# Optimization experiments

Measured on AMD Instinct MI355X. Metric: run time of the kernel, lower is better.

The kernel has to match this reference:

```python
import jax, jax.numpy as jnp
import numpy as np

B, S, H = 64, 2048, 1024

def setup_inputs() -> dict:
    key = jax.random.key(0)
    k1, k2, k3, k4, k5 = jax.random.split(key, 5)
    scale = 1.0 / np.sqrt(H)
    return {
        "dec_hidden": jax.random.normal(k1, (B, 1, H), dtype=jnp.float32),
        "enc_outputs": jax.random.normal(k2, (B, S, H), dtype=jnp.float32),
        "W_h": jax.random.normal(k3, (H, H), dtype=jnp.float32) * scale,
        "W_s": jax.random.normal(k4, (H, H), dtype=jnp.float32) * scale,
        "v": jax.random.normal(k5, (H,), dtype=jnp.float32) * scale,
    }

def reference(dec_hidden, enc_outputs, W_h, W_s, v):
    # energy = tanh(enc @ W_h^T + dec @ W_s^T)  -> [B, S, H]
    enc_proj = jnp.einsum('bsh,oh->bso', enc_outputs, W_h)
    dec_proj = jnp.einsum('bqh,oh->bqo', dec_hidden, W_s)  # [B,1,H]
    energy = jnp.tanh(enc_proj + dec_proj)
    # score = energy @ v -> [B, S]
    score = jnp.einsum('bsh,h->bs', energy, v)
    weights = jax.nn.softmax(score, axis=-1)
    # context = weights[:, None, :] @ enc_outputs -> [B, 1, H]
    context = jnp.einsum('bs,bsh->bh', weights, enc_outputs)[:, None, :]
    return (context, weights)
```

## Files before the change

kernel.cpp:

```cpp
#include <hip/hip_runtime.h>
#include <hip/hip_bf16.h>


#define B_ 64
#define S_ 2048
#define H_ 1024
#define NT_ 16

typedef __attribute__((ext_vector_type(8))) short short8;
typedef __attribute__((ext_vector_type(4))) float floatx4;

__device__ __forceinline__ short f2bf(float f) {
    unsigned u = __float_as_uint(f);
    return (short)((u + 0x7FFFu + ((u >> 16) & 1u)) >> 16);
}
__device__ __forceinline__ unsigned pk2bf(float a, float b) {
    unsigned ua = __float_as_uint(a), ub = __float_as_uint(b);
    ua = (ua + 0x7FFFu + ((ua >> 16) & 1u)) >> 16;
    ub = (ub + 0x7FFFu + ((ub >> 16) & 1u)) & 0xFFFF0000u;
    return ua | ub;
}
__device__ __forceinline__ void gload_lds16(const void* g, void* l) {
    __builtin_amdgcn_global_load_lds(
        (const __attribute__((address_space(1))) unsigned*)g,
        (__attribute__((address_space(3))) unsigned*)l, 16, 0, 0);
}

__global__ __launch_bounds__(256) void zero_score_kernel(float* __restrict__ sc) {
    ((float4*)sc)[blockIdx.x * 256 + threadIdx.x] = make_float4(0.f, 0.f, 0.f, 0.f);
}

__global__ __launch_bounds__(256) void dec_proj_kernel(
        const float* __restrict__ dec, const float* __restrict__ Ws,
        float* __restrict__ dp) {
    __shared__ float sdec[H_];
    const int b = blockIdx.y;
    const int o = blockIdx.x * 256 + threadIdx.x;
    ((float4*)sdec)[threadIdx.x] = ((const float4*)(dec + b * H_))[threadIdx.x];
    __syncthreads();
    const float4* wr = (const float4*)(Ws + (size_t)o * H_);
    float acc = 0.f;
#pragma unroll 4
    for (int i = 0; i < H_ / 4; ++i) {
        float4 wv = wr[i];
        acc += sdec[4*i+0]*wv.x + sdec[4*i+1]*wv.y + sdec[4*i+2]*wv.z + sdec[4*i+3]*wv.w;
    }
    dp[b * H_ + o] = acc;
}

__global__ __launch_bounds__(256) void cvt_wh_kernel(
        const float* __restrict__ Wh, short* __restrict__ Wbf) {
    const int i = blockIdx.x * 256 + threadIdx.x;
    float4 f = ((const float4*)Wh)[i];
    *(short4*)&Wbf[i * 4] = make_short4(f2bf(f.x), f2bf(f.y), f2bf(f.z), f2bf(f.w));
}

__global__ __launch_bounds__(256) void cvt_enc_kernel(
        const float* __restrict__ enc, short* __restrict__ out) {
    const size_t total = (size_t)B_ * S_ * H_ / 8;
    for (size_t c = (size_t)blockIdx.x * 256 + threadIdx.x; c < total;
         c += (size_t)gridDim.x * 256) {
        const float4* p = (const float4*)enc + c * 2;
        float4 f0 = p[0], f1 = p[1];
        union { short8 s; unsigned u[4]; } cv;
        cv.u[0] = pk2bf(f0.x, f0.y);
        cv.u[1] = pk2bf(f0.z, f0.w);
        cv.u[2] = pk2bf(f1.x, f1.y);
        cv.u[3] = pk2bf(f1.z, f1.w);
        ((short8*)out)[c] = cv.s;
    }
}

#define STAGEA(bufp, half, ktile) do {                                          \
    gload_lds16(gA + (size_t)(half) * (128 * H_) + (ktile) * 64,                \
                &As[(bufp)][(half)][wave * 512]);                               \
    gload_lds16(gA + (size_t)(half) * (128 * H_) + (ktile) * 64 + 64 * H_,      \
                &As[(bufp)][(half)][4096 + wave * 512]);                        \
} while (0)
#define STAGEB(bufp, half, ktile) do {                                          \
    gload_lds16(gB + (size_t)(half) * (128 * H_) + (ktile) * 64,                \
                &Bs[(bufp)][(half)][wave * 512]);                               \
    gload_lds16(gB + (size_t)(half) * (128 * H_) + (ktile) * 64 + 64 * H_,      \
                &Bs[(bufp)][(half)][4096 + wave * 512]);                        \
} while (0)

#define MFMA16(I0) do {                                                         \
    _Pragma("unroll")                                                           \
    for (int kt = 0; kt < 2; ++kt) {                                            \
        _Pragma("unroll")                                                       \
        for (int j = 0; j < 4; ++j) {                                           \
            acc[I0][j]     = __builtin_amdgcn_mfma_f32_16x16x32_bf16(           \
                                 af[0][kt], bfr[kt][j], acc[I0][j], 0, 0, 0);   \
            acc[(I0)+1][j] = __builtin_amdgcn_mfma_f32_16x16x32_bf16(           \
                                 af[1][kt], bfr[kt][j], acc[(I0)+1][j], 0, 0, 0); \
        }                                                                       \
    }                                                                           \
} while (0)

#define PHASE(I0, STG, TAILWAIT) do {                                           \
    _Pragma("unroll")                                                           \
    for (int ii = 0; ii < 2; ++ii)                                              \
        _Pragma("unroll")                                                       \
        for (int kt = 0; kt < 2; ++kt)                                          \
            af[ii][kt] = *(const short8*)(aBase + ((I0) + ii) * 1024 +          \
                                          (((kt * 4 + quad) ^ swz) * 8));       \
    STG;                                                                        \
    __builtin_amdgcn_s_barrier();                                               \
    asm volatile("s_waitcnt lgkmcnt(0)" ::: "memory");                          \
    __builtin_amdgcn_s_setprio(1);                                              \
    MFMA16(I0);                                                                 \
    __builtin_amdgcn_s_setprio(0);                                              \
    TAILWAIT;                                                                   \
    __builtin_amdgcn_s_barrier();                                               \
} while (0)

__global__ __launch_bounds__(512, 2) void score256_kernel(
        const short* __restrict__ encbf, const short* __restrict__ Wbf,
        const float* __restrict__ dp, const float* __restrict__ v,
        float* __restrict__ score) {
    __shared__ short As[2][2][128 * 64];
    __shared__ short Bs[2][2][128 * 64];

    const int tid  = threadIdx.x;
    const int wave = tid >> 6;
    const int lane = tid & 63;
    const int l15  = lane & 15;
    const int quad = lane >> 4;
    const int wy   = wave & 1;
    const int wx   = wave >> 1;

    const int mtile = blockIdx.x >> 2;
    const int nb    = blockIdx.x & 3;
    const int m0    = mtile * 256;
    const int n0    = nb * 256;
    const int b     = m0 >> 11;
    const int swz   = l15 & 7;

    const int rr0 = tid >> 3;
    const int g8  = (tid & 7) ^ (rr0 & 7);
    const short* gA = encbf + (size_t)(m0 + rr0) * H_ + g8 * 8;
    const short* gB = Wbf   + (size_t)(n0 + rr0) * H_ + g8 * 8;

    floatx4 acc[8][4];
#pragma unroll
    for (int i = 0; i < 8; ++i)
#pragma unroll
        for (int j = 0; j < 4; ++j) acc[i][j] = (floatx4){0.f, 0.f, 0.f, 0.f};

    short8 af[2][2];
    short8 bfr[2][4];

    STAGEA(0, 0, 0); STAGEA(0, 1, 0);
    STAGEB(0, 0, 0); STAGEB(0, 1, 0);
    STAGEB(1, 0, 1); STAGEB(1, 1, 1);
    asm volatile("s_waitcnt vmcnt(4)" ::: "memory");
    __builtin_amdgcn_s_barrier();

#pragma unroll 1
    for (int t = 0; t < NT_; ++t) {
        const int buf = t & 1;
        const short* aBase = &As[buf][wy][0] + l15 * 64;
        const short* bBase = &Bs[buf][wx >> 1][0] + ((wx & 1) * 64 + l15) * 64;

#pragma unroll
        for (int kt = 0; kt < 2; ++kt)
#pragma unroll
            for (int j = 0; j < 4; ++j)
                bfr[kt][j] = *(const short8*)(bBase + j * 1024 +
                                              (((kt * 4 + quad) ^ swz) * 8));

        PHASE(0, { if (t + 1 < NT_) STAGEA(buf ^ 1, 0, t + 1); }, (void)0);
        PHASE(2, { if (t + 1 < NT_) STAGEA(buf ^ 1, 1, t + 1); }, (void)0);
        PHASE(4, { if (t + 2 < NT_) STAGEB(buf, 0, t + 2); }, (void)0);
        PHASE(6, { if (t + 2 < NT_) STAGEB(buf, 1, t + 2); },
              { if (t < NT_ - 2) { asm volatile("s_waitcnt vmcnt(4)" ::: "memory"); }
                else             { asm volatile("s_waitcnt vmcnt(0)" ::: "memory"); } });
    }

    float part[8][4];
#pragma unroll
    for (int i = 0; i < 8; ++i)
#pragma unroll
        for (int r = 0; r < 4; ++r) part[i][r] = 0.f;

#pragma unroll
    for (int j = 0; j < 4; ++j) {
        const int o = n0 + wx * 64 + j * 16 + l15;
        const float dpv = dp[b * H_ + o];
        const float vv  = v[o];
#pragma unroll
        for (int i = 0; i < 8; ++i)
#pragma unroll
            for (int r = 0; r < 4; ++r) {
                float x = acc[i][j][r] + dpv;
                x = fminf(10.f, fmaxf(-10.f, x));
                float e = __expf(x + x);
                float t = 1.f - 2.f * __builtin_amdgcn_rcpf(e + 1.f);
                part[i][r] += t * vv;
            }
    }
#pragma unroll
    for (int i = 0; i < 8; ++i)
#pragma unroll
        for (int r = 0; r < 4; ++r) {
            float s = part[i][r];
            s += __shfl_xor(s, 1, 64);
            s += __shfl_xor(s, 2, 64);
            s += __shfl_xor(s, 4, 64);
            s += __shfl_xor(s, 8, 64);
            if (l15 == 0)
                atomicAdd(&score[m0 + wy * 128 + i * 16 + quad * 4 + r], s);
        }
}

__global__ __launch_bounds__(256, 3) void score_kernel_fb(
        const float* __restrict__ enc, const short* __restrict__ Wbf,
        const float* __restrict__ dp, const float* __restrict__ v,
        float* __restrict__ score) {
    __shared__ short As[128 * 64];
    __shared__ short Bs[128 * 64];

    const int tid  = threadIdx.x;
    const int wave = tid >> 6;
    const int lane = tid & 63;
    const int l15  = lane & 15;
    const int quad = lane >> 4;
    const int wy   = wave & 1;
    const int wx   = wave >> 1;

    const int mtile = blockIdx.x >> 3;
    const int nb    = blockIdx.x & 7;
    const int m0    = mtile * 128;
    const int n0    = nb * 128;
    const int b     = m0 >> 11;

    floatx4 acc[4][4];
#pragma unroll
    for (int i = 0; i < 4; ++i)
#pragma unroll
        for (int j = 0; j < 4; ++j) acc[i][j] = (floatx4){0.f, 0.f, 0.f, 0.f};

    const short* aLds = As + (wy * 64 + l15) * 64;
    const short* bLds = Bs + (wx * 64 + l15) * 64;
    const int swz = l15 & 7;
    const int srow = tid >> 3;
    const int bc   = tid & 7;

    for (int k0 = 0; k0 < H_; k0 += 64) {
#pragma unroll
        for (int r = 0; r < 4; ++r) {
            const int n = r * 32 + srow;
            const int g = bc ^ (n & 7);
            const short* gp = Wbf + (size_t)(n0 + n) * H_ + k0 + g * 8;
            gload_lds16(gp, (void*)(Bs + (r * 256 + wave * 64) * 8));
        }
#pragma unroll
        for (int i = 0; i < 4; ++i) {
            const int La = i * 256 + tid;
            const int m  = La >> 3;
            const int c8 = La & 7;
            const float4* gp = (const float4*)(enc + (size_t)(m0 + m) * H_ + k0 + c8 * 8);
            float4 f0 = gp[0], f1 = gp[1];
            union { short8 s; unsigned u[4]; } cv;
            cv.u[0] = pk2bf(f0.x, f0.y);
            cv.u[1] = pk2bf(f0.z, f0.w);
            cv.u[2] = pk2bf(f1.x, f1.y);
            cv.u[3] = pk2bf(f1.z, f1.w);
            *(short8*)&As[m * 64 + (c8 ^ (m & 7)) * 8] = cv.s;
        }
        __syncthreads();
#pragma unroll
        for (int kt = 0; kt < 2; ++kt) {
            short8 a2[4], b2[4];
#pragma unroll
            for (int i = 0; i < 4; ++i)
                a2[i] = *(const short8*)(aLds + i * 16 * 64 + (((kt * 4 + quad) ^ swz) * 8));
#pragma unroll
            for (int j = 0; j < 4; ++j)
                b2[j] = *(const short8*)(bLds + j * 16 * 64 + (((kt * 4 + quad) ^ swz) * 8));
#pragma unroll
            for (int i = 0; i < 4; ++i)
#pragma unroll
                for (int j = 0; j < 4; ++j)
                    acc[i][j] = __builtin_amdgcn_mfma_f32_16x16x32_bf16(a2[i], b2[j], acc[i][j], 0, 0, 0);
        }
        __syncthreads();
    }

    float part[4][4];
#pragma unroll
    for (int i = 0; i < 4; ++i)
#pragma unroll
        for (int r = 0; r < 4; ++r) part[i][r] = 0.f;
#pragma unroll
    for (int j = 0; j < 4; ++j) {
        const int o = n0 + wx * 64 + j * 16 + l15;
        const float dpv = dp[b * H_ + o];
        const float vv  = v[o];
#pragma unroll
        for (int i = 0; i < 4; ++i)
#pragma unroll
            for (int r = 0; r < 4; ++r) {
                float x = acc[i][j][r] + dpv;
                x = fminf(10.f, fmaxf(-10.f, x));
                float e = __expf(x + x);
                float t = 1.f - 2.f * __builtin_amdgcn_rcpf(e + 1.f);
                part[i][r] += t * vv;
            }
    }
#pragma unroll
    for (int i = 0; i < 4; ++i)
#pragma unroll
        for (int r = 0; r < 4; ++r) {
            float s = part[i][r];
            s += __shfl_xor(s, 1, 64);
            s += __shfl_xor(s, 2, 64);
            s += __shfl_xor(s, 4, 64);
            s += __shfl_xor(s, 8, 64);
            if (l15 == 0)
                atomicAdd(&score[m0 + wy * 64 + i * 16 + quad * 4 + r], s);
        }
}

__global__ __launch_bounds__(256) void softmax_kernel(float* __restrict__ out) {
    const int b = blockIdx.x;
    const int tid = threadIdx.x;
    float* sc = out + B_ * H_ + b * S_;

    ((float4*)(out + b * H_))[tid] = make_float4(0.f, 0.f, 0.f, 0.f);

    float xs[8];
    float m = -1e30f;
#pragma unroll
    for (int i = 0; i < 8; ++i) { xs[i] = sc[tid + i * 256]; m = fmaxf(m, xs[i]); }
#pragma unroll
    for (int off = 32; off > 0; off >>= 1) m = fmaxf(m, __shfl_xor(m, off, 64));
    __shared__ float redm[4];
    const int wv = tid >> 6;
    if ((tid & 63) == 0) redm[wv] = m;
    __syncthreads();
    m = fmaxf(fmaxf(redm[0], redm[1]), fmaxf(redm[2], redm[3]));

    float s = 0.f;
#pragma unroll
    for (int i = 0; i < 8; ++i) { xs[i] = __expf(xs[i] - m); s += xs[i]; }
#pragma unroll
    for (int off = 32; off > 0; off >>= 1) s += __shfl_xor(s, off, 64);
    __shared__ float reds[4];
    if ((tid & 63) == 0) reds[wv] = s;
    __syncthreads();
    s = reds[0] + reds[1] + reds[2] + reds[3];

    const float inv = 1.f / s;
#pragma unroll
    for (int i = 0; i < 8; ++i) sc[tid + i * 256] = xs[i] * inv;
}

__global__ __launch_bounds__(256) void context_kernel(
        const float* __restrict__ enc, const float* __restrict__ wts,
        float* __restrict__ ctx) {
    const int b    = blockIdx.x;
    const int scnk = blockIdx.y;
    const int t    = threadIdx.x;
    const float* w  = wts + b * S_ + scnk * 256;
    const float4* e = (const float4*)(enc + ((long)b * S_ + scnk * 256) * H_);
    float4 acc = make_float4(0.f, 0.f, 0.f, 0.f);
#pragma unroll 4
    for (int s = 0; s < 256; ++s) {
        const float ww = w[s];
        const float4 ev = e[s * (H_ / 4) + t];
        acc.x = fmaf(ww, ev.x, acc.x);
        acc.y = fmaf(ww, ev.y, acc.y);
        acc.z = fmaf(ww, ev.z, acc.z);
        acc.w = fmaf(ww, ev.w, acc.w);
    }
    float* c = ctx + b * H_ + t * 4;
    atomicAdd(c + 0, acc.x);
    atomicAdd(c + 1, acc.y);
    atomicAdd(c + 2, acc.z);
    atomicAdd(c + 3, acc.w);
}

extern "C" void kernel_launch(void* const* d_in, const int* in_sizes, int n_in,
                              void* d_out, int out_size, void* d_ws, size_t ws_size,
                              hipStream_t stream) {
    const float* dec = (const float*)d_in[0];
    const float* enc = (const float*)d_in[1];
    const float* Wh  = (const float*)d_in[2];
    const float* Ws  = (const float*)d_in[3];
    const float* v   = (const float*)d_in[4];

    float* out = (float*)d_out;
    float* ctx = out;
    float* wts = out + B_ * H_;

    float* dp  = (float*)d_ws;
    short* Wbf = (short*)((char*)d_ws + (size_t)B_ * H_ * 4);
    const size_t base = (size_t)B_ * H_ * 4 + (size_t)H_ * H_ * 2;
    const size_t enc_need = (size_t)B_ * S_ * H_ * 2;
    short* encbf = (ws_size >= base + enc_need)
                       ? (short*)((char*)d_ws + base) : nullptr;
    (void)in_sizes; (void)n_in; (void)out_size;

    zero_score_kernel<<<(B_ * S_ / 4) / 256, 256, 0, stream>>>(wts);
    dec_proj_kernel<<<dim3(H_ / 256, B_), 256, 0, stream>>>(dec, Ws, dp);
    cvt_wh_kernel<<<(H_ * H_ / 4) / 256, 256, 0, stream>>>(Wh, Wbf);
    if (encbf) {
        cvt_enc_kernel<<<8192, 256, 0, stream>>>(enc, encbf);
        score256_kernel<<<(B_ * S_ / 256) * (H_ / 256), 512, 0, stream>>>(
            encbf, Wbf, dp, v, wts);
    } else {
        score_kernel_fb<<<(B_ * S_ / 128) * (H_ / 128), 256, 0, stream>>>(
            enc, Wbf, dp, v, wts);
    }
    softmax_kernel<<<B_, 256, 0, stream>>>(out);
    context_kernel<<<dim3(B_, S_ / 256), 256, 0, stream>>>(enc, wts, ctx);
}
```

Before: 1.198 ms.

## Switch score GEMM to 32x32x16 MFMA tiles and remap block order

```diff
diff --git a/kernel.cpp b/kernel.cpp
--- a/kernel.cpp
+++ b/kernel.cpp
@@ -9,6 +9,7 @@
 
 typedef __attribute__((ext_vector_type(8))) short short8;
 typedef __attribute__((ext_vector_type(4))) float floatx4;
+typedef __attribute__((ext_vector_type(16))) float floatx16;
 
 __device__ __forceinline__ short f2bf(float f) {
     unsigned u = __float_as_uint(f);
@@ -84,31 +85,22 @@
                 &Bs[(bufp)][(half)][4096 + wave * 512]);                        \
 } while (0)
 
-#define MFMA16(I0) do {                                                         \
-    _Pragma("unroll")                                                           \
-    for (int kt = 0; kt < 2; ++kt) {                                            \
-        _Pragma("unroll")                                                       \
-        for (int j = 0; j < 4; ++j) {                                           \
-            acc[I0][j]     = __builtin_amdgcn_mfma_f32_16x16x32_bf16(           \
-                                 af[0][kt], bfr[kt][j], acc[I0][j], 0, 0, 0);   \
-            acc[(I0)+1][j] = __builtin_amdgcn_mfma_f32_16x16x32_bf16(           \
-                                 af[1][kt], bfr[kt][j], acc[(I0)+1][j], 0, 0, 0); \
-        }                                                                       \
-    }                                                                           \
-} while (0)
-
 #define PHASE(I0, STG, TAILWAIT) do {                                           \
     _Pragma("unroll")                                                           \
-    for (int ii = 0; ii < 2; ++ii)                                              \
-        _Pragma("unroll")                                                       \
-        for (int kt = 0; kt < 2; ++kt)                                          \
-            af[ii][kt] = *(const short8*)(aBase + ((I0) + ii) * 1024 +          \
-                                          (((kt * 4 + quad) ^ swz) * 8));       \
+    for (int kt = 0; kt < 4; ++kt)                                              \
+        af[kt] = *(const short8*)(aBase + (I0) * 2048 +                         \
+                                  (((kt * 2 + lhi) ^ swz) * 8));                \
     STG;                                                                        \
     __builtin_amdgcn_s_barrier();                                               \
     asm volatile("s_waitcnt lgkmcnt(0)" ::: "memory");                          \
     __builtin_amdgcn_s_setprio(1);                                              \
-    MFMA16(I0);                                                                 \
+    _Pragma("unroll")                                                           \
+    for (int kt = 0; kt < 4; ++kt) {                                            \
+        acc[I0][0] = __builtin_amdgcn_mfma_f32_32x32x16_bf16(                   \
+                         af[kt], bfr[kt][0], acc[I0][0], 0, 0, 0);              \
+        acc[I0][1] = __builtin_amdgcn_mfma_f32_32x32x16_bf16(                   \
+                         af[kt], bfr[kt][1], acc[I0][1], 0, 0, 0);              \
+    }                                                                           \
     __builtin_amdgcn_s_setprio(0);                                              \
     TAILWAIT;                                                                   \
     __builtin_amdgcn_s_barrier();                                               \
@@ -124,31 +116,34 @@
     const int tid  = threadIdx.x;
     const int wave = tid >> 6;
     const int lane = tid & 63;
-    const int l15  = lane & 15;
-    const int quad = lane >> 4;
+    const int l31  = lane & 31;
+    const int lhi  = lane >> 5;
     const int wy   = wave & 1;
     const int wx   = wave >> 1;
 
-    const int mtile = blockIdx.x >> 2;
-    const int nb    = blockIdx.x & 3;
+    const int wid   = ((blockIdx.x & 7) << 8) | (blockIdx.x >> 3);
+    const int mtile = wid >> 2;
+    const int nb    = wid & 3;
     const int m0    = mtile * 256;
     const int n0    = nb * 256;
     const int b     = m0 >> 11;
-    const int swz   = l15 & 7;
+    const int swz   = lane & 7;
 
     const int rr0 = tid >> 3;
     const int g8  = (tid & 7) ^ (rr0 & 7);
     const short* gA = encbf + (size_t)(m0 + rr0) * H_ + g8 * 8;
     const short* gB = Wbf   + (size_t)(n0 + rr0) * H_ + g8 * 8;
 
-    floatx4 acc[8][4];
-#pragma unroll
-    for (int i = 0; i < 8; ++i)
-#pragma unroll
-        for (int j = 0; j < 4; ++j) acc[i][j] = (floatx4){0.f, 0.f, 0.f, 0.f};
-
-    short8 af[2][2];
-    short8 bfr[2][4];
+    floatx16 acc[4][2];
+#pragma unroll
+    for (int i = 0; i < 4; ++i)
+#pragma unroll
+        for (int j = 0; j < 2; ++j)
+#pragma unroll
+            for (int r = 0; r < 16; ++r) acc[i][j][r] = 0.f;
+
+    short8 af[4];
+    short8 bfr[4][2];
 
     STAGEA(0, 0, 0); STAGEA(0, 1, 0);
     STAGEB(0, 0, 0); STAGEB(0, 1, 0);
@@ -159,58 +154,60 @@
 #pragma unroll 1
     for (int t = 0; t < NT_; ++t) {
         const int buf = t & 1;
-        const short* aBase = &As[buf][wy][0] + l15 * 64;
-        const short* bBase = &Bs[buf][wx >> 1][0] + ((wx & 1) * 64 + l15) * 64;
-
-#pragma unroll
-        for (int kt = 0; kt < 2; ++kt)
-#pragma unroll
-            for (int j = 0; j < 4; ++j)
-                bfr[kt][j] = *(const short8*)(bBase + j * 1024 +
-                                              (((kt * 4 + quad) ^ swz) * 8));
+        const short* aBase = &As[buf][wy][0] + l31 * 64;
+        const short* bBase = &Bs[buf][wx >> 1][0] + ((wx & 1) * 64 + l31) * 64;
+
+#pragma unroll
+        for (int kt = 0; kt < 4; ++kt)
+#pragma unroll
+            for (int j = 0; j < 2; ++j)
+                bfr[kt][j] = *(const short8*)(bBase + j * 2048 +
+                                              (((kt * 2 + lhi) ^ swz) * 8));
 
         PHASE(0, { if (t + 1 < NT_) STAGEA(buf ^ 1, 0, t + 1); }, (void)0);
-        PHASE(2, { if (t + 1 < NT_) STAGEA(buf ^ 1, 1, t + 1); }, (void)0);
-        PHASE(4, { if (t + 2 < NT_) STAGEB(buf, 0, t + 2); }, (void)0);
-        PHASE(6, { if (t + 2 < NT_) STAGEB(buf, 1, t + 2); },
+        PHASE(1, { if (t + 1 < NT_) STAGEA(buf ^ 1, 1, t + 1); }, (void)0);
+        PHASE(2, { if (t + 2 < NT_) STAGEB(buf, 0, t + 2); }, (void)0);
+        PHASE(3, { if (t + 2 < NT_) STAGEB(buf, 1, t + 2); },
               { if (t < NT_ - 2) { asm volatile("s_waitcnt vmcnt(4)" ::: "memory"); }
                 else             { asm volatile("s_waitcnt vmcnt(0)" ::: "memory"); } });
     }
 
-    float part[8][4];
-#pragma unroll
-    for (int i = 0; i < 8; ++i)
-#pragma unroll
-        for (int r = 0; r < 4; ++r) part[i][r] = 0.f;
-
-#pragma unroll
-    for (int j = 0; j < 4; ++j) {
-        const int o = n0 + wx * 64 + j * 16 + l15;
-        const float dpv = dp[b * H_ + o];
-        const float vv  = v[o];
-#pragma unroll
-        for (int i = 0; i < 8; ++i)
-#pragma unroll
-            for (int r = 0; r < 4; ++r) {
-                float x = acc[i][j][r] + dpv;
+    float dpv[2], vv2[2];
+#pragma unroll
+    for (int j = 0; j < 2; ++j) {
+        const int o = n0 + wx * 64 + j * 32 + l31;
+        dpv[j] = dp[b * H_ + o];
+        vv2[j] = v[o];
+    }
+#pragma unroll
+    for (int i = 0; i < 4; ++i) {
+        float p[16];
+#pragma unroll
+        for (int r = 0; r < 16; ++r) p[r] = 0.f;
+#pragma unroll
+        for (int j = 0; j < 2; ++j) {
+#pragma unroll
+            for (int r = 0; r < 16; ++r) {
+                float x = acc[i][j][r] + dpv[j];
                 x = fminf(10.f, fmaxf(-10.f, x));
                 float e = __expf(x + x);
                 float t = 1.f - 2.f * __builtin_amdgcn_rcpf(e + 1.f);
-                part[i][r] += t * vv;
+                p[r] += t * vv2[j];
             }
-    }
-#pragma unroll
-    for (int i = 0; i < 8; ++i)
-#pragma unroll
-        for (int r = 0; r < 4; ++r) {
-            float s = part[i][r];
+        }
+#pragma unroll
+        for (int r = 0; r < 16; ++r) {
+            float s = p[r];
             s += __shfl_xor(s, 1, 64);
             s += __shfl_xor(s, 2, 64);
             s += __shfl_xor(s, 4, 64);
             s += __shfl_xor(s, 8, 64);
-            if (l15 == 0)
-                atomicAdd(&score[m0 + wy * 128 + i * 16 + quad * 4 + r], s);
-        }
+            s += __shfl_xor(s, 16, 64);
+            if (l31 == 0)
+                atomicAdd(&score[m0 + wy * 128 + i * 32 +
+                                 (r & 3) + 8 * (r >> 2) + lhi * 4], s);
+        }
+    }
 }
 
 __global__ __launch_bounds__(256, 3) void score_kernel_fb(
```

After: 1.321 ms. +10.3%, slower.
